# Kernel optimization log

Measured on AMD Instinct MI355X. Metric: run time of the kernel, lower is better.

## Reference

```python
import jax, jax.numpy as jnp
import numpy as np

BN_EPS = 1e-5
NUM_GC_LAYERS = 3
NUM_LAYERS = NUM_GC_LAYERS + 4  # 7
N_NODES = 50000
N_EDGES = 600000
DIM = 128


def setup_inputs() -> dict:
    key = jax.random.key(0)
    ks = jax.random.split(key, 9)
    x = jax.random.normal(ks[0], (N_NODES, DIM), dtype=jnp.float32)
    edge_index = jax.random.randint(ks[1], (2, N_EDGES), 0, N_NODES, dtype=jnp.int64)
    batch = jnp.zeros((N_NODES,), dtype=jnp.int64)
    s = 0.1
    W1 = jax.random.normal(ks[2], (NUM_LAYERS, DIM, DIM), dtype=jnp.float32) * s
    b1 = jax.random.normal(ks[3], (NUM_LAYERS, DIM), dtype=jnp.float32) * s
    W2 = jax.random.normal(ks[4], (NUM_LAYERS, DIM, DIM), dtype=jnp.float32) * s
    b2 = jax.random.normal(ks[5], (NUM_LAYERS, DIM), dtype=jnp.float32) * s
    gamma = jnp.ones((NUM_LAYERS, DIM), dtype=jnp.float32)
    beta = jnp.zeros((NUM_LAYERS, DIM), dtype=jnp.float32)
    return {"x": x, "edge_index": edge_index, "batch": batch,
            "W1": W1, "b1": b1, "W2": W2, "b2": b2,
            "gamma": gamma, "beta": beta}


def _gin_conv(x, src, dst, W1, b1, W2, b2):
    # GINConv with eps=0: out = MLP(x + sum_{j in N(i)} x_j)
    agg = jax.ops.segment_sum(x[src], dst, num_segments=x.shape[0])  # [N, D]
    h = x + agg
    h = jnp.maximum(h @ W1 + b1, 0.0) @ W2 + b2
    return h


def _batch_norm(h, g, b):
    # BatchNorm1d in training mode: biased batch stats over nodes
    mean = jnp.mean(h, axis=0)
    var = jnp.var(h, axis=0)
    return (h - mean) * jax.lax.rsqrt(var + BN_EPS) * g + b


def reference(x, edge_index, batch, W1, b1, W2, b2, gamma, beta):
    src, dst = edge_index[0], edge_index[1]
    for i in range(NUM_GC_LAYERS):
        h = _gin_conv(x, src, dst, W1[i], b1[i], W2[i], b2[i])
        x = _batch_norm(jnp.maximum(h, 0.0), gamma[i], beta[i])
    j = NUM_GC_LAYERS
    outs = []
    for k in range(j, j + 4):
        h = _gin_conv(x, src, dst, W1[k], b1[k], W2[k], b2[k])
        outs.append(_batch_norm(jnp.tanh(h), gamma[k], beta[k]))
    return tuple(outs)
```

## Files before the change

kernel.cpp:

```cpp
#include <hip/hip_runtime.h>
#include <math.h>

#define NN 50000
#define NE 600000
#define DIM 128
#define NLAYERS 7
#define LDK 136
#define BN_EPS 1e-5f
#define GB 782
#define PART_SLOT 200192

typedef __attribute__((ext_vector_type(4))) float floatx4;
typedef __attribute__((ext_vector_type(8))) _Float16 half8;
typedef __attribute__((ext_vector_type(2))) _Float16 half2v;

__device__ __forceinline__ unsigned short f2h(float f) {
  _Float16 h = (_Float16)f;
  return __builtin_bit_cast(unsigned short, h);
}
__device__ __forceinline__ float2 up(unsigned int u) {
  half2v h = __builtin_bit_cast(half2v, u);
  return make_float2((float)h.x, (float)h.y);
}
__device__ __forceinline__ unsigned int pk(float a, float b) {
  half2v h;
  h.x = (_Float16)a;
  h.y = (_Float16)b;
  return __builtin_bit_cast(unsigned int, h);
}
__device__ __forceinline__ float tanh_fast(float x) {
  float e = __expf(2.0f * x);
  return 1.0f - 2.0f * __builtin_amdgcn_rcpf(e + 1.0f);
}


__global__ void hist_kernel(const int* __restrict__ ei, int* __restrict__ deg) {
  int e = blockIdx.x * 256 + threadIdx.x;
  if (e < NE) atomicAdd(&deg[ei[NE + e]], 1);
}

__global__ __launch_bounds__(256) void scan_part(const int* __restrict__ deg,
                                                 int* __restrict__ rowl,
                                                 int* __restrict__ bsum) {
  int b = blockIdx.x, t = threadIdx.x;
  int base = b * 1024 + t * 4;
  int d[4];
  #pragma unroll
  for (int j = 0; j < 4; j++) d[j] = (base + j < NN) ? deg[base + j] : 0;
  int s = d[0] + d[1] + d[2] + d[3];
  int lane = t & 63;
  int incl = s;
  #pragma unroll
  for (int off = 1; off < 64; off <<= 1) {
    int n = __shfl_up(incl, off);
    if (lane >= off) incl += n;
  }
  __shared__ int wtot[4];
  if (lane == 63) wtot[t >> 6] = incl;
  __syncthreads();
  int woff = 0;
  for (int w = 0; w < (t >> 6); w++) woff += wtot[w];
  int run = woff + incl - s;
  #pragma unroll
  for (int j = 0; j < 4; j++) {
    if (base + j < NN) rowl[base + j] = run;
    run += d[j];
  }
  if (t == 255) bsum[b] = woff + incl;
}

__global__ void scan_top(const int* __restrict__ bsum, int* __restrict__ boff,
                         int* __restrict__ row) {
  int t = threadIdx.x;
  int v = (t < 49) ? bsum[t] : 0;
  int incl = v;
  #pragma unroll
  for (int off = 1; off < 64; off <<= 1) {
    int n = __shfl_up(incl, off);
    if (t >= off) incl += n;
  }
  if (t < 49) boff[t] = incl - v;
  if (t == 48) row[NN] = incl;
}

__global__ __launch_bounds__(256) void scan_apply(const int* __restrict__ rowl,
                                                  const int* __restrict__ boff,
                                                  int* __restrict__ row,
                                                  int* __restrict__ cur) {
  int i = blockIdx.x * 256 + threadIdx.x;
  if (i < NN) {
    int r = rowl[i] + boff[i >> 10];
    row[i] = r;
    cur[i] = r;
  }
}

__global__ void bucket_kernel(const int* __restrict__ ei, int* __restrict__ cur,
                              int* __restrict__ esrc) {
  int e = blockIdx.x * 256 + threadIdx.x;
  if (e < NE) {
    int d = ei[NE + e];
    int p = atomicAdd(&cur[d], 1);
    esrc[p] = ei[e];
  }
}


__global__ void convw_kernel(const float* __restrict__ W1, const float* __restrict__ W2,
                             unsigned short* __restrict__ wb) {
  int i = blockIdx.x * 256 + threadIdx.x;
  if (i >= NLAYERS * 16384) return;
  int l = i >> 14;
  int r = i & 16383;
  int n = r >> 7;
  int k = r & 127;
  wb[(size_t)(l * 2 + 0) * 16384 + n * 128 + k] = f2h(W1[(size_t)l * 16384 + k * 128 + n]);
  wb[(size_t)(l * 2 + 1) * 16384 + n * 128 + k] = f2h(W2[(size_t)l * 16384 + k * 128 + n]);
}

__global__ __launch_bounds__(256) void convx_kernel(const float* __restrict__ x,
                                                    unsigned int* __restrict__ x16) {
  int i = blockIdx.x * 256 + threadIdx.x;
  float4 v = ((const float4*)x)[i];
  uint2 o;
  o.x = pk(v.x, v.y);
  o.y = pk(v.z, v.w);
  ((uint2*)x16)[i] = o;
}


__global__ __launch_bounds__(256) void gather_kernel(
    const unsigned int* __restrict__ x16, const int* __restrict__ esrc,
    const int* __restrict__ row, unsigned int* __restrict__ agg16) {
  int w = (blockIdx.x * 256 + threadIdx.x) >> 6;
  int lane = threadIdx.x & 63;
  if (w >= NN) return;
  int s0 = row[w], s1 = row[w + 1];
  float ax = 0.f, ay = 0.f;
  int e = s0;
  for (; e + 7 < s1; e += 8) {
    int idx[8];
    #pragma unroll
    for (int j = 0; j < 8; j++) idx[j] = esrc[e + j];
    unsigned int v[8];
    #pragma unroll
    for (int j = 0; j < 8; j++) v[j] = x16[idx[j] * 64 + lane];
    #pragma unroll
    for (int j = 0; j < 8; j++) {
      float2 f = up(v[j]);
      ax += f.x;
      ay += f.y;
    }
  }
  for (; e + 3 < s1; e += 4) {
    int i0 = esrc[e], i1 = esrc[e + 1], i2 = esrc[e + 2], i3 = esrc[e + 3];
    unsigned int v0 = x16[i0 * 64 + lane];
    unsigned int v1 = x16[i1 * 64 + lane];
    unsigned int v2 = x16[i2 * 64 + lane];
    unsigned int v3 = x16[i3 * 64 + lane];
    float2 f0 = up(v0), f1 = up(v1), f2 = up(v2), f3 = up(v3);
    ax += (f0.x + f1.x) + (f2.x + f3.x);
    ay += (f0.y + f1.y) + (f2.y + f3.y);
  }
  for (; e < s1; e++) {
    float2 f = up(x16[esrc[e] * 64 + lane]);
    ax += f.x;
    ay += f.y;
  }
  agg16[w * 64 + lane] = pk(ax, ay);
}


__global__ __launch_bounds__(256) void mlp1_kernel(
    const unsigned int* __restrict__ x16, const unsigned int* __restrict__ agg16,
    const unsigned short* __restrict__ wb,
    const float* __restrict__ b1, const float* __restrict__ b2,
    unsigned short* __restrict__ xout16, float* __restrict__ part,
    const float* __restrict__ bnPrev, const float* __restrict__ gPrev,
    const float* __restrict__ btPrev, const int* __restrict__ deg, int hasPrev) {
  __shared__ unsigned short hS[64 * LDK];
  __shared__ unsigned short wS[128 * LDK];
  __shared__ float scshS[256];
  int tid = threadIdx.x;
  int row0 = blockIdx.x * 64;

  if (tid < 128) {
    float sc = 1.f, sh = 0.f;
    if (hasPrev) {
      const float inv = 1.f / (float)NN;
      float mean = bnPrev[tid] * inv;
      float var = bnPrev[128 + tid] * inv - mean * mean;
      sc = gPrev[tid] * rsqrtf(var + BN_EPS);
      sh = btPrev[tid] - mean * sc;
    }
    scshS[tid] = sc;
    scshS[128 + tid] = sh;
  }
  __syncthreads();

  for (int idx = tid; idx < 1024; idx += 256) {
    int r = idx >> 4;
    int c = (idx & 15) * 8;
    uint4 hv = {0u, 0u, 0u, 0u};
    if (row0 + r < NN) {
      size_t base = (size_t)(row0 + r) * 16 + (c >> 3);
      uint4 xv = ((const uint4*)x16)[base];
      uint4 av = ((const uint4*)agg16)[base];
      float dr = 1.f + (float)deg[row0 + r];
      unsigned int xs[4] = {xv.x, xv.y, xv.z, xv.w};
      unsigned int as_[4] = {av.x, av.y, av.z, av.w};
      unsigned int hs[4];
      #pragma unroll
      for (int j = 0; j < 4; j++) {
        float2 xf = up(xs[j]);
        float2 af = up(as_[j]);
        int cc = c + j * 2;
        float h0 = scshS[cc] * (xf.x + af.x) + dr * scshS[128 + cc];
        float h1 = scshS[cc + 1] * (xf.y + af.y) + dr * scshS[128 + cc + 1];
        hs[j] = pk(h0, h1);
      }
      hv.x = hs[0]; hv.y = hs[1]; hv.z = hs[2]; hv.w = hs[3];
    }
    *(uint4*)&hS[r * LDK + c] = hv;
  }
  for (int q = tid; q < 2048; q += 256) {
    int rw = q >> 4;
    int c8 = (q & 15) * 8;
    *(uint4*)&wS[rw * LDK + c8] = *(const uint4*)(wb + rw * 128 + c8);
  }
  __syncthreads();

  int lane = tid & 63;
  int wav = tid >> 6;
  int quad = lane >> 4;
  int lm = lane & 15;
  int mrow = wav * 16 + lm;

  floatx4 acc[8];
  #pragma unroll
  for (int nt = 0; nt < 8; nt++) {
    float bv = b1[nt * 16 + lm];
    floatx4 c = {bv, bv, bv, bv};
    #pragma unroll
    for (int ks = 0; ks < 4; ks++) {
      half8 af = *(half8*)&hS[mrow * LDK + ks * 32 + quad * 8];
      half8 bf = *(half8*)&wS[(nt * 16 + lm) * LDK + ks * 32 + quad * 8];
      c = __builtin_amdgcn_mfma_f32_16x16x32_f16(af, bf, c, 0, 0, 0);
    }
    acc[nt] = c;
  }
  #pragma unroll
  for (int nt = 0; nt < 8; nt++) {
    #pragma unroll
    for (int rg = 0; rg < 4; rg++) {
      float v = acc[nt][rg];
      v = v > 0.f ? v : 0.f;
      hS[(wav * 16 + quad * 4 + rg) * LDK + nt * 16 + lm] = f2h(v);
    }
  }
  __syncthreads();
  for (int q = tid; q < 2048; q += 256) {
    int rw = q >> 4;
    int c8 = (q & 15) * 8;
    *(uint4*)&wS[rw * LDK + c8] = *(const uint4*)(wb + 16384 + rw * 128 + c8);
  }
  __syncthreads();

  bool wvalid = (row0 + wav * 16) < NN;
  float sArr[8], sqArr[8];
  #pragma unroll
  for (int nt = 0; nt < 8; nt++) {
    float bv = b2[nt * 16 + lm];
    floatx4 c = {bv, bv, bv, bv};
    #pragma unroll
    for (int ks = 0; ks < 4; ks++) {
      half8 af = *(half8*)&hS[mrow * LDK + ks * 32 + quad * 8];
      half8 bf = *(half8*)&wS[(nt * 16 + lm) * LDK + ks * 32 + quad * 8];
      c = __builtin_amdgcn_mfma_f32_16x16x32_f16(af, bf, c, 0, 0, 0);
    }
    float s = 0.f, sq = 0.f;
    #pragma unroll
    for (int rg = 0; rg < 4; rg++) {
      float v = c[rg];
      v = v > 0.f ? v : 0.f;
      if (wvalid)
        xout16[(size_t)(row0 + wav * 16 + quad * 4 + rg) * DIM + nt * 16 + lm] = f2h(v);
      s += v;
      sq += v * v;
    }
    s += __shfl_xor(s, 16);
    s += __shfl_xor(s, 32);
    sq += __shfl_xor(sq, 16);
    sq += __shfl_xor(sq, 32);
    sArr[nt] = s;
    sqArr[nt] = sq;
  }
  __syncthreads();
  float* redS = (float*)hS;
  if (quad == 0) {
    #pragma unroll
    for (int nt = 0; nt < 8; nt++) {
      redS[wav * 256 + nt * 16 + lm] = wvalid ? sArr[nt] : 0.f;
      redS[wav * 256 + 128 + nt * 16 + lm] = wvalid ? sqArr[nt] : 0.f;
    }
  }
  __syncthreads();
  float v = redS[tid] + redS[256 + tid] + redS[512 + tid] + redS[768 + tid];
  part[(size_t)blockIdx.x * 256 + tid] = v;
}


__global__ __launch_bounds__(256) void mlp4_kernel(
    const unsigned int* __restrict__ x16, const unsigned int* __restrict__ agg16,
    const unsigned short* __restrict__ wbg,
    const float* __restrict__ b1g, const float* __restrict__ b2g,
    float* __restrict__ out, float* __restrict__ partBase,
    const float* __restrict__ bnPrev, const float* __restrict__ gPrev,
    const float* __restrict__ btPrev, const int* __restrict__ deg) {
  __shared__ unsigned short hS[64 * LDK];
  __shared__ unsigned short wS[128 * LDK];
  __shared__ float scshS[256];
  int tid = threadIdx.x;
  int row0 = blockIdx.x * 64;

  if (tid < 128) {
    const float inv = 1.f / (float)NN;
    float mean = bnPrev[tid] * inv;
    float var = bnPrev[128 + tid] * inv - mean * mean;
    float sc = gPrev[tid] * rsqrtf(var + BN_EPS);
    scshS[tid] = sc;
    scshS[128 + tid] = btPrev[tid] - mean * sc;
  }
  __syncthreads();

  for (int idx = tid; idx < 1024; idx += 256) {
    int r = idx >> 4;
    int c = (idx & 15) * 8;
    uint4 hv = {0u, 0u, 0u, 0u};
    if (row0 + r < NN) {
      size_t base = (size_t)(row0 + r) * 16 + (c >> 3);
      uint4 xv = ((const uint4*)x16)[base];
      uint4 av = ((const uint4*)agg16)[base];
      float dr = 1.f + (float)deg[row0 + r];
      unsigned int xs[4] = {xv.x, xv.y, xv.z, xv.w};
      unsigned int as_[4] = {av.x, av.y, av.z, av.w};
      unsigned int hs[4];
      #pragma unroll
      for (int j = 0; j < 4; j++) {
        float2 xf = up(xs[j]);
        float2 af = up(as_[j]);
        int cc = c + j * 2;
        float h0 = scshS[cc] * (xf.x + af.x) + dr * scshS[128 + cc];
        float h1 = scshS[cc + 1] * (xf.y + af.y) + dr * scshS[128 + cc + 1];
        hs[j] = pk(h0, h1);
      }
      hv.x = hs[0]; hv.y = hs[1]; hv.z = hs[2]; hv.w = hs[3];
    }
    *(uint4*)&hS[r * LDK + c] = hv;
  }
  __syncthreads();

  int lane = tid & 63;
  int wav = tid >> 6;
  int quad = lane >> 4;
  int lm = lane & 15;
  int mrow = wav * 16 + lm;
  bool wvalid = (row0 + wav * 16) < NN;

  half8 aF[4];
  #pragma unroll
  for (int ks = 0; ks < 4; ks++)
    aF[ks] = *(half8*)&hS[mrow * LDK + ks * 32 + quad * 8];

  #pragma unroll 1
  for (int ly = 0; ly < 4; ly++) {
    int layer = 3 + ly;
    const unsigned short* wb = wbg + (size_t)layer * 2 * 16384;
    const float* b1 = b1g + layer * 128;
    const float* b2 = b2g + layer * 128;
    float* act = out + (size_t)ly * NN * DIM;
    float* part = partBase + (size_t)ly * PART_SLOT;

    __syncthreads();
    for (int q = tid; q < 2048; q += 256) {
      int rw = q >> 4;
      int c8 = (q & 15) * 8;
      *(uint4*)&wS[rw * LDK + c8] = *(const uint4*)(wb + rw * 128 + c8);
    }
    __syncthreads();

    floatx4 acc[8];
    #pragma unroll
    for (int nt = 0; nt < 8; nt++) {
      float bv = b1[nt * 16 + lm];
      floatx4 c = {bv, bv, bv, bv};
      #pragma unroll
      for (int ks = 0; ks < 4; ks++) {
        half8 bf = *(half8*)&wS[(nt * 16 + lm) * LDK + ks * 32 + quad * 8];
        c = __builtin_amdgcn_mfma_f32_16x16x32_f16(aF[ks], bf, c, 0, 0, 0);
      }
      acc[nt] = c;
    }
    #pragma unroll
    for (int nt = 0; nt < 8; nt++) {
      #pragma unroll
      for (int rg = 0; rg < 4; rg++) {
        float v = acc[nt][rg];
        v = v > 0.f ? v : 0.f;
        hS[(wav * 16 + quad * 4 + rg) * LDK + nt * 16 + lm] = f2h(v);
      }
    }
    __syncthreads();
    for (int q = tid; q < 2048; q += 256) {
      int rw = q >> 4;
      int c8 = (q & 15) * 8;
      *(uint4*)&wS[rw * LDK + c8] = *(const uint4*)(wb + 16384 + rw * 128 + c8);
    }
    __syncthreads();

    float sArr[8], sqArr[8];
    #pragma unroll
    for (int nt = 0; nt < 8; nt++) {
      float bv = b2[nt * 16 + lm];
      floatx4 c = {bv, bv, bv, bv};
      #pragma unroll
      for (int ks = 0; ks < 4; ks++) {
        half8 af = *(half8*)&hS[mrow * LDK + ks * 32 + quad * 8];
        half8 bf = *(half8*)&wS[(nt * 16 + lm) * LDK + ks * 32 + quad * 8];
        c = __builtin_amdgcn_mfma_f32_16x16x32_f16(af, bf, c, 0, 0, 0);
      }
      float s = 0.f, sq = 0.f;
      #pragma unroll
      for (int rg = 0; rg < 4; rg++) {
        float v = c[rg];
        v = tanh_fast(v);
        if (wvalid)
          act[(size_t)(row0 + wav * 16 + quad * 4 + rg) * DIM + nt * 16 + lm] = v;
        s += v;
        sq += v * v;
      }
      s += __shfl_xor(s, 16);
      s += __shfl_xor(s, 32);
      sq += __shfl_xor(sq, 16);
      sq += __shfl_xor(sq, 32);
      sArr[nt] = s;
      sqArr[nt] = sq;
    }
    __syncthreads();
    float* redS = (float*)hS;
    if (quad == 0) {
      #pragma unroll
      for (int nt = 0; nt < 8; nt++) {
        redS[wav * 256 + nt * 16 + lm] = wvalid ? sArr[nt] : 0.f;
        redS[wav * 256 + 128 + nt * 16 + lm] = wvalid ? sqArr[nt] : 0.f;
      }
    }
    __syncthreads();
    float v = redS[tid] + redS[256 + tid] + redS[512 + tid] + redS[768 + tid];
    part[(size_t)blockIdx.x * 256 + tid] = v;
  }
}


__global__ __launch_bounds__(256) void reduce_kernel(const float* __restrict__ part,
                                                     float* __restrict__ bn) {
  int c = blockIdx.x;
  int t = threadIdx.x;
  const float* p = part + (size_t)blockIdx.y * PART_SLOT + c;
  float s = 0.f;
  for (int b = t; b < GB; b += 256) s += p[(size_t)b * 256];
  #pragma unroll
  for (int off = 1; off < 64; off <<= 1) s += __shfl_xor(s, off);
  __shared__ float wsum[4];
  if ((t & 63) == 0) wsum[t >> 6] = s;
  __syncthreads();
  if (t == 0) bn[blockIdx.y * 256 + c] = wsum[0] + wsum[1] + wsum[2] + wsum[3];
}


__global__ __launch_bounds__(256) void norm_kernel(
    const float* __restrict__ aBase, const float* __restrict__ bnAll,
    const float* __restrict__ gammaAll, const float* __restrict__ betaAll,
    float* __restrict__ oBase, int layer0) {
  int layer = layer0 + blockIdx.y;
  const float* a = aBase + (size_t)blockIdx.y * NN * DIM;
  const float* bn = bnAll + blockIdx.y * 256;
  const float* gamma = gammaAll + layer * 128;
  const float* beta = betaAll + layer * 128;
  float* o = oBase + (size_t)blockIdx.y * NN * DIM;
  int i = blockIdx.x * 256 + threadIdx.x;
  int f = (i & 31) * 4;
  const float inv = 1.f / (float)NN;
  float4 v = ((const float4*)a)[i];
  float r[4] = {v.x, v.y, v.z, v.w};
  #pragma unroll
  for (int j = 0; j < 4; j++) {
    float mean = bn[f + j] * inv;
    float var = bn[128 + f + j] * inv - mean * mean;
    float sc = gamma[f + j] * rsqrtf(var + BN_EPS);
    r[j] = (r[j] - mean) * sc + beta[f + j];
  }
  float4 ov; ov.x = r[0]; ov.y = r[1]; ov.z = r[2]; ov.w = r[3];
  ((float4*)o)[i] = ov;
}


extern "C" void kernel_launch(void* const* d_in, const int* in_sizes, int n_in,
                              void* d_out, int out_size, void* d_ws, size_t ws_size,
                              hipStream_t stream) {
  const float* x_in = (const float*)d_in[0];
  const int* ei = (const int*)d_in[1];
  const float* W1g = (const float*)d_in[3];
  const float* b1g = (const float*)d_in[4];
  const float* W2g = (const float*)d_in[5];
  const float* b2g = (const float*)d_in[6];
  const float* gg = (const float*)d_in[7];
  const float* bg = (const float*)d_in[8];
  float* out = (float*)d_out;

  char* ws = (char*)d_ws;
  const size_t OFF_X16 = 0;
  const size_t OFF_A16 = 12800000;
  const size_t OFF_WB = 25600000;
  const size_t OFF_BN = 26058752;
  const size_t OFF_DEG = 26062848;
  const size_t OFF_ROW = 26262848;
  const size_t OFF_CUR = 26462852;
  const size_t OFF_ESR = 26662852;
  const size_t OFF_PART = 29062852;

  unsigned int* X16 = (unsigned int*)(ws + OFF_X16);
  unsigned int* A16 = (unsigned int*)(ws + OFF_A16);
  unsigned short* wb = (unsigned short*)(ws + OFF_WB);
  float* bn = (float*)(ws + OFF_BN);
  int* deg = (int*)(ws + OFF_DEG);
  int* rowp = (int*)(ws + OFF_ROW);
  int* cur = (int*)(ws + OFF_CUR);
  int* esrc = (int*)(ws + OFF_ESR);
  float* part = (float*)(ws + OFF_PART);
  int* rowl = (int*)(ws + OFF_PART);
  int* bsum = (int*)(ws + OFF_PART + 800000);
  int* boff = (int*)(ws + OFF_PART + 800256);

  hipMemsetAsync(deg, 0, NN * sizeof(int), stream);
  hist_kernel<<<(NE + 255) / 256, 256, 0, stream>>>(ei, deg);
  scan_part<<<49, 256, 0, stream>>>(deg, rowl, bsum);
  scan_top<<<1, 64, 0, stream>>>(bsum, boff, rowp);
  scan_apply<<<196, 256, 0, stream>>>(rowl, boff, rowp, cur);
  bucket_kernel<<<(NE + 255) / 256, 256, 0, stream>>>(ei, cur, esrc);
  convw_kernel<<<(NLAYERS * 16384 + 255) / 256, 256, 0, stream>>>(W1g, W2g, wb);
  convx_kernel<<<NN * DIM / 4 / 256, 256, 0, stream>>>(x_in, X16);

  for (int i = 0; i < 3; i++) {
    gather_kernel<<<(NN * 64 + 255) / 256, 256, 0, stream>>>(X16, esrc, rowp, A16);
    mlp1_kernel<<<GB, 256, 0, stream>>>(
        X16, A16, wb + (size_t)i * 2 * 16384, b1g + i * 128, b2g + i * 128,
        (unsigned short*)X16, part,
        (i == 0) ? bn : bn + (i - 1) * 256,
        (i == 0) ? gg : gg + (i - 1) * 128,
        (i == 0) ? bg : bg + (i - 1) * 128, deg, i > 0 ? 1 : 0);
    reduce_kernel<<<dim3(256, 1), 256, 0, stream>>>(part, bn + i * 256);
  }
  gather_kernel<<<(NN * 64 + 255) / 256, 256, 0, stream>>>(X16, esrc, rowp, A16);
  mlp4_kernel<<<GB, 256, 0, stream>>>(X16, A16, wb, b1g, b2g, out, part,
                                      bn + 2 * 256, gg + 2 * 128, bg + 2 * 128, deg);
  reduce_kernel<<<dim3(256, 4), 256, 0, stream>>>(part, bn);
  norm_kernel<<<dim3(NN * DIM / 4 / 256, 4), 256, 0, stream>>>(out, bn, gg, bg, out, 3);
}
```

Measured before the change: 493.2 us.

## Fuse neighbor gather into MLP kernels with ping-pong feature buffers

Result: slower. 653.0 us (+32.4%).

```diff
diff --git a/kernel.cpp b/kernel.cpp
--- a/kernel.cpp
+++ b/kernel.cpp
@@ -129,55 +129,14 @@
 }
 
 
-__global__ __launch_bounds__(256) void gather_kernel(
-    const unsigned int* __restrict__ x16, const int* __restrict__ esrc,
-    const int* __restrict__ row, unsigned int* __restrict__ agg16) {
-  int w = (blockIdx.x * 256 + threadIdx.x) >> 6;
-  int lane = threadIdx.x & 63;
-  if (w >= NN) return;
-  int s0 = row[w], s1 = row[w + 1];
-  float ax = 0.f, ay = 0.f;
-  int e = s0;
-  for (; e + 7 < s1; e += 8) {
-    int idx[8];
-    #pragma unroll
-    for (int j = 0; j < 8; j++) idx[j] = esrc[e + j];
-    unsigned int v[8];
-    #pragma unroll
-    for (int j = 0; j < 8; j++) v[j] = x16[idx[j] * 64 + lane];
-    #pragma unroll
-    for (int j = 0; j < 8; j++) {
-      float2 f = up(v[j]);
-      ax += f.x;
-      ay += f.y;
-    }
-  }
-  for (; e + 3 < s1; e += 4) {
-    int i0 = esrc[e], i1 = esrc[e + 1], i2 = esrc[e + 2], i3 = esrc[e + 3];
-    unsigned int v0 = x16[i0 * 64 + lane];
-    unsigned int v1 = x16[i1 * 64 + lane];
-    unsigned int v2 = x16[i2 * 64 + lane];
-    unsigned int v3 = x16[i3 * 64 + lane];
-    float2 f0 = up(v0), f1 = up(v1), f2 = up(v2), f3 = up(v3);
-    ax += (f0.x + f1.x) + (f2.x + f3.x);
-    ay += (f0.y + f1.y) + (f2.y + f3.y);
-  }
-  for (; e < s1; e++) {
-    float2 f = up(x16[esrc[e] * 64 + lane]);
-    ax += f.x;
-    ay += f.y;
-  }
-  agg16[w * 64 + lane] = pk(ax, ay);
-}
-
-
 __global__ __launch_bounds__(256) void mlp1_kernel(
-    const unsigned int* __restrict__ x16, const unsigned int* __restrict__ agg16,
+    const unsigned int* __restrict__ xin16, unsigned short* __restrict__ xout16,
+    const int* __restrict__ rowp, const int* __restrict__ esrc,
     const unsigned short* __restrict__ wb,
     const float* __restrict__ b1, const float* __restrict__ b2,
-    unsigned short* __restrict__ xout16, float* __restrict__ part,
+    float* __restrict__ part,
     const float* __restrict__ bnPrev, const float* __restrict__ gPrev,
-    const float* __restrict__ btPrev, const int* __restrict__ deg, int hasPrev) {
+    const float* __restrict__ btPrev, int hasPrev) {
   __shared__ unsigned short hS[64 * LDK];
   __shared__ unsigned short wS[128 * LDK];
   __shared__ float scshS[256];
@@ -198,43 +157,81 @@
   }
   __syncthreads();
 
-  for (int idx = tid; idx < 1024; idx += 256) {
-    int r = idx >> 4;
-    int c = (idx & 15) * 8;
-    uint4 hv = {0u, 0u, 0u, 0u};
-    if (row0 + r < NN) {
-      size_t base = (size_t)(row0 + r) * 16 + (c >> 3);
-      uint4 xv = ((const uint4*)x16)[base];
-      uint4 av = ((const uint4*)agg16)[base];
-      float dr = 1.f + (float)deg[row0 + r];
-      unsigned int xs[4] = {xv.x, xv.y, xv.z, xv.w};
-      unsigned int as_[4] = {av.x, av.y, av.z, av.w};
-      unsigned int hs[4];
-      #pragma unroll
-      for (int j = 0; j < 4; j++) {
-        float2 xf = up(xs[j]);
-        float2 af = up(as_[j]);
-        int cc = c + j * 2;
-        float h0 = scshS[cc] * (xf.x + af.x) + dr * scshS[128 + cc];
-        float h1 = scshS[cc + 1] * (xf.y + af.y) + dr * scshS[128 + cc + 1];
-        hs[j] = pk(h0, h1);
-      }
-      hv.x = hs[0]; hv.y = hs[1]; hv.z = hs[2]; hv.w = hs[3];
-    }
-    *(uint4*)&hS[r * LDK + c] = hv;
-  }
-  for (int q = tid; q < 2048; q += 256) {
-    int rw = q >> 4;
-    int c8 = (q & 15) * 8;
-    *(uint4*)&wS[rw * LDK + c8] = *(const uint4*)(wb + rw * 128 + c8);
-  }
-  __syncthreads();
-
   int lane = tid & 63;
   int wav = tid >> 6;
+
+  uint4 wreg[8];
+  #pragma unroll
+  for (int j = 0; j < 8; j++) {
+    int q = tid + j * 256;
+    wreg[j] = *(const uint4*)(wb + (q >> 4) * 128 + (q & 15) * 8);
+  }
+
+  float sc0 = scshS[lane * 2], sc1 = scshS[lane * 2 + 1];
+  float sh0 = scshS[128 + lane * 2], sh1 = scshS[128 + lane * 2 + 1];
+
+  int nodeBase = row0 + wav * 16;
+  for (int t = 0; t < 16; t++) {
+    int n = nodeBase + t;
+    bool nv = n < NN;
+    int s0 = 0, s1 = 0;
+    if (nv) { s0 = rowp[n]; s1 = rowp[n + 1]; }
+    unsigned int xv = nv ? xin16[(size_t)n * 64 + lane] : 0u;
+    float ax = 0.f, ay = 0.f;
+    int e = s0;
+    for (; e + 7 < s1; e += 8) {
+      int idx[8];
+      #pragma unroll
+      for (int j = 0; j < 8; j++) idx[j] = esrc[e + j];
+      unsigned int v[8];
+      #pragma unroll
+      for (int j = 0; j < 8; j++) v[j] = xin16[(size_t)idx[j] * 64 + lane];
+      #pragma unroll
+      for (int j = 0; j < 8; j++) {
+        float2 f = up(v[j]);
+        ax += f.x;
+        ay += f.y;
+      }
+    }
+    for (; e + 3 < s1; e += 4) {
+      int i0 = esrc[e], i1 = esrc[e + 1], i2 = esrc[e + 2], i3 = esrc[e + 3];
+      unsigned int v0 = xin16[(size_t)i0 * 64 + lane];
+      unsigned int v1 = xin16[(size_t)i1 * 64 + lane];
+      unsigned int v2 = xin16[(size_t)i2 * 64 + lane];
+      unsigned int v3 = xin16[(size_t)i3 * 64 + lane];
+      float2 f0 = up(v0), f1 = up(v1), f2 = up(v2), f3 = up(v3);
+      ax += (f0.x + f1.x) + (f2.x + f3.x);
+      ay += (f0.y + f1.y) + (f2.y + f3.y);
+    }
+    for (; e < s1; e++) {
+      float2 f = up(xin16[(size_t)esrc[e] * 64 + lane]);
+      ax += f.x;
+      ay += f.y;
+    }
+    float2 xf = up(xv);
+    float dr = 1.f + (float)(s1 - s0);
+    float h0 = sc0 * (xf.x + ax) + dr * sh0;
+    float h1 = sc1 * (xf.y + ay) + dr * sh1;
+    unsigned int hw = nv ? pk(h0, h1) : 0u;
+    *(unsigned int*)&hS[(wav * 16 + t) * LDK + lane * 2] = hw;
+  }
+
+  #pragma unroll
+  for (int j = 0; j < 8; j++) {
+    int q = tid + j * 256;
+    *(uint4*)&wS[(q >> 4) * LDK + (q & 15) * 8] = wreg[j];
+  }
+  __syncthreads();
+
   int quad = lane >> 4;
   int lm = lane & 15;
   int mrow = wav * 16 + lm;
+  bool wvalid = (row0 + wav * 16) < NN;
+
+  half8 aF[4];
+  #pragma unroll
+  for (int ks = 0; ks < 4; ks++)
+    aF[ks] = *(half8*)&hS[mrow * LDK + ks * 32 + quad * 8];
 
   floatx4 acc[8];
   #pragma unroll
@@ -243,9 +240,8 @@
     floatx4 c = {bv, bv, bv, bv};
     #pragma unroll
     for (int ks = 0; ks < 4; ks++) {
-      half8 af = *(half8*)&hS[mrow * LDK + ks * 32 + quad * 8];
       half8 bf = *(half8*)&wS[(nt * 16 + lm) * LDK + ks * 32 + quad * 8];
-      c = __builtin_amdgcn_mfma_f32_16x16x32_f16(af, bf, c, 0, 0, 0);
+      c = __builtin_amdgcn_mfma_f32_16x16x32_f16(aF[ks], bf, c, 0, 0, 0);
     }
     acc[nt] = c;
   }
@@ -266,7 +262,6 @@
   }
   __syncthreads();
 
-  bool wvalid = (row0 + wav * 16) < NN;
   float sArr[8], sqArr[8];
   #pragma unroll
   for (int nt = 0; nt < 8; nt++) {
@@ -311,12 +306,13 @@
 
 
 __global__ __launch_bounds__(256) void mlp4_kernel(
-    const unsigned int* __restrict__ x16, const unsigned int* __restrict__ agg16,
+    const unsigned int* __restrict__ xin16,
+    const int* __restrict__ rowp, const int* __restrict__ esrc,
     const unsigned short* __restrict__ wbg,
     const float* __restrict__ b1g, const float* __restrict__ b2g,
     float* __restrict__ out, float* __restrict__ partBase,
     const float* __restrict__ bnPrev, const float* __restrict__ gPrev,
-    const float* __restrict__ btPrev, const int* __restrict__ deg) {
+    const float* __restrict__ btPrev) {
   __shared__ unsigned short hS[64 * LDK];
   __shared__ unsigned short wS[128 * LDK];
   __shared__ float scshS[256];
@@ -333,35 +329,58 @@
   }
   __syncthreads();
 
-  for (int idx = tid; idx < 1024; idx += 256) {
-    int r = idx >> 4;
-    int c = (idx & 15) * 8;
-    uint4 hv = {0u, 0u, 0u, 0u};
-    if (row0 + r < NN) {
-      size_t base = (size_t)(row0 + r) * 16 + (c >> 3);
-      uint4 xv = ((const uint4*)x16)[base];
-      uint4 av = ((const uint4*)agg16)[base];
-      float dr = 1.f + (float)deg[row0 + r];
-      unsigned int xs[4] = {xv.x, xv.y, xv.z, xv.w};
-      unsigned int as_[4] = {av.x, av.y, av.z, av.w};
-      unsigned int hs[4];
-      #pragma unroll
-      for (int j = 0; j < 4; j++) {
-        float2 xf = up(xs[j]);
-        float2 af = up(as_[j]);
-        int cc = c + j * 2;
-        float h0 = scshS[cc] * (xf.x + af.x) + dr * scshS[128 + cc];
-        float h1 = scshS[cc + 1] * (xf.y + af.y) + dr * scshS[128 + cc + 1];
-        hs[j] = pk(h0, h1);
-      }
-      hv.x = hs[0]; hv.y = hs[1]; hv.z = hs[2]; hv.w = hs[3];
-    }
-    *(uint4*)&hS[r * LDK + c] = hv;
-  }
-  __syncthreads();
-
   int lane = tid & 63;
   int wav = tid >> 6;
+
+  float sc0 = scshS[lane * 2], sc1 = scshS[lane * 2 + 1];
+  float sh0 = scshS[128 + lane * 2], sh1 = scshS[128 + lane * 2 + 1];
+
+  int nodeBase = row0 + wav * 16;
+  for (int t = 0; t < 16; t++) {
+    int n = nodeBase + t;
+    bool nv = n < NN;
+    int s0 = 0, s1 = 0;
+    if (nv) { s0 = rowp[n]; s1 = rowp[n + 1]; }
+    unsigned int xv = nv ? xin16[(size_t)n * 64 + lane] : 0u;
+    float ax = 0.f, ay = 0.f;
+    int e = s0;
+    for (; e + 7 < s1; e += 8) {
+      int idx[8];
+      #pragma unroll
+      for (int j = 0; j < 8; j++) idx[j] = esrc[e + j];
+      unsigned int v[8];
+      #pragma unroll
+      for (int j = 0; j < 8; j++) v[j] = xin16[(size_t)idx[j] * 64 + lane];
+      #pragma unroll
+      for (int j = 0; j < 8; j++) {
+        float2 f = up(v[j]);
+        ax += f.x;
+        ay += f.y;
+      }
+    }
+    for (; e + 3 < s1; e += 4) {
+      int i0 = esrc[e], i1 = esrc[e + 1], i2 = esrc[e + 2], i3 = esrc[e + 3];
+      unsigned int v0 = xin16[(size_t)i0 * 64 + lane];
+      unsigned int v1 = xin16[(size_t)i1 * 64 + lane];
+      unsigned int v2 = xin16[(size_t)i2 * 64 + lane];
+      unsigned int v3 = xin16[(size_t)i3 * 64 + lane];
+      float2 f0 = up(v0), f1 = up(v1), f2 = up(v2), f3 = up(v3);
+      ax += (f0.x + f1.x) + (f2.x + f3.x);
+      ay += (f0.y + f1.y) + (f2.y + f3.y);
+    }
+    for (; e < s1; e++) {
+      float2 f = up(xin16[(size_t)esrc[e] * 64 + lane]);
+      ax += f.x;
+      ay += f.y;
+    }
+    float2 xf = up(xv);
+    float dr = 1.f + (float)(s1 - s0);
+    float h0 = sc0 * (xf.x + ax) + dr * sh0;
+    float h1 = sc1 * (xf.y + ay) + dr * sh1;
+    unsigned int hw = nv ? pk(h0, h1) : 0u;
+    *(unsigned int*)&hS[(wav * 16 + t) * LDK + lane * 2] = hw;
+  }
+
   int quad = lane >> 4;
   int lm = lane & 15;
   int mrow = wav * 16 + lm;
@@ -519,8 +538,8 @@
   float* out = (float*)d_out;
 
   char* ws = (char*)d_ws;
-  const size_t OFF_X16 = 0;
-  const size_t OFF_A16 = 12800000;
+  const size_t OFF_XA = 0;
+  const size_t OFF_XB = 12800000;
   const size_t OFF_WB = 25600000;
   const size_t OFF_BN = 26058752;
   const size_t OFF_DEG = 26062848;
@@ -529,8 +548,8 @@
   const size_t OFF_ESR = 26662852;
   const size_t OFF_PART = 29062852;
 
-  unsigned int* X16 = (unsigned int*)(ws + OFF_X16);
-  unsigned int* A16 = (unsigned int*)(ws + OFF_A16);
+  unsigned int* X16a = (unsigned int*)(ws + OFF_XA);
+  unsigned int* X16b = (unsigned int*)(ws + OFF_XB);
   unsigned short* wb = (unsigned short*)(ws + OFF_WB);
   float* bn = (float*)(ws + OFF_BN);
   int* deg = (int*)(ws + OFF_DEG);
@@ -549,21 +568,22 @@
   scan_apply<<<196, 256, 0, stream>>>(rowl, boff, rowp, cur);
   bucket_kernel<<<(NE + 255) / 256, 256, 0, stream>>>(ei, cur, esrc);
   convw_kernel<<<(NLAYERS * 16384 + 255) / 256, 256, 0, stream>>>(W1g, W2g, wb);
-  convx_kernel<<<NN * DIM / 4 / 256, 256, 0, stream>>>(x_in, X16);
-
+  convx_kernel<<<NN * DIM / 4 / 256, 256, 0, stream>>>(x_in, X16a);
+
+  unsigned int* xin = X16a;
+  unsigned int* xout = X16b;
   for (int i = 0; i < 3; i++) {
-    gather_kernel<<<(NN * 64 + 255) / 256, 256, 0, stream>>>(X16, esrc, rowp, A16);
     mlp1_kernel<<<GB, 256, 0, stream>>>(
-        X16, A16, wb + (size_t)i * 2 * 16384, b1g + i * 128, b2g + i * 128,
-        (unsigned short*)X16, part,
+        xin, (unsigned short*)xout, rowp, esrc,
+        wb + (size_t)i * 2 * 16384, b1g + i * 128, b2g + i * 128, part,
         (i == 0) ? bn : bn + (i - 1) * 256,
         (i == 0) ? gg : gg + (i - 1) * 128,
-        (i == 0) ? bg : bg + (i - 1) * 128, deg, i > 0 ? 1 : 0);
+        (i == 0) ? bg : bg + (i - 1) * 128, i > 0 ? 1 : 0);
     reduce_kernel<<<dim3(256, 1), 256, 0, stream>>>(part, bn + i * 256);
-  }
-  gather_kernel<<<(NN * 64 + 255) / 256, 256, 0, stream>>>(X16, esrc, rowp, A16);
-  mlp4_kernel<<<GB, 256, 0, stream>>>(X16, A16, wb, b1g, b2g, out, part,
-                                      bn + 2 * 256, gg + 2 * 128, bg + 2 * 128, deg);
+    unsigned int* tmp = xin; xin = xout; xout = tmp;
+  }
+  mlp4_kernel<<<GB, 256, 0, stream>>>(xin, rowp, esrc, wb, b1g, b2g, out, part,
+                                      bn + 2 * 256, gg + 2 * 128, bg + 2 * 128);
   reduce_kernel<<<dim3(256, 4), 256, 0, stream>>>(part, bn);
   norm_kernel<<<dim3(NN * DIM / 4 / 256, 4), 256, 0, stream>>>(out, bn, gg, bg, out, 3);
 }
```
